# Kernel optimization log

Measured on AMD Instinct MI355X. Metric: run time of the kernel, lower is better.

Reference implementation:

```python
import jax, jax.numpy as jnp
import numpy as np

N, C, S = 2, 512, 256
SCALE = 2.0

def setup_inputs() -> dict:
    key = jax.random.key(0)
    kq, kk, kv = jax.random.split(key, 3)
    q = jax.random.normal(kq, (N, C, S), dtype=jnp.float32)
    k = jax.random.normal(kk, (N, C, S), dtype=jnp.float32)
    v = jax.random.normal(kv, (N, C, S), dtype=jnp.float32)
    return {"q": q, "k": k, "v": v}

def reference(q, k, v):
    # q: (N,C,S) -> (N,C,1,S); k: (N,C,S) -> (N,1,C,S)
    # weights[n,c,d] = -sum_s |k[n,d,s] - q[n,c,s]| / scale
    diff = jnp.abs(k[:, None, :, :] - q[:, :, None, :])  # (N,C,C,S)
    weights = -(diff / SCALE).sum(axis=-1)               # (N,C,C)
    weights = jax.nn.softmax(weights, axis=-1)
    rep = jnp.einsum('ncd,nds->ncs', weights, v)         # (N,C,S)
    return rep
```

## Files before the change

kernel.cpp:

```cpp
#include <hip/hip_runtime.h>
#include <hip/hip_bf16.h>


constexpr int N_ = 2;
constexpr int C_ = 512;
constexpr int S_ = 256;
constexpr int TC = 4;
constexpr int NW = 4;

template <int CTRL, int ROW_MASK>
__device__ __forceinline__ float dpp_add(float x) {
    int yi = __builtin_amdgcn_update_dpp(0, __float_as_int(x), CTRL, ROW_MASK, 0xf, true);
    return x + __int_as_float(yi);
}
template <int CTRL, int ROW_MASK>
__device__ __forceinline__ float dpp_max(float x) {
    int yi = __builtin_amdgcn_update_dpp(__float_as_int(x), __float_as_int(x), CTRL, ROW_MASK, 0xf, false);
    return fmaxf(x, __int_as_float(yi));
}
__device__ __forceinline__ float dpp_reduce_halves(float x) {
    x = dpp_add<0x111, 0xf>(x);
    x = dpp_add<0x112, 0xf>(x);
    x = dpp_add<0x114, 0xf>(x);
    x = dpp_add<0x118, 0xf>(x);
    x = dpp_add<0x142, 0xa>(x);
    return x;
}
__device__ __forceinline__ float wave_sum_bcast(float x) {
    x = dpp_reduce_halves(x);
    x = dpp_add<0x143, 0xc>(x);
    return __int_as_float(__builtin_amdgcn_readlane(__float_as_int(x), 63));
}
__device__ __forceinline__ float wave_max_bcast(float x) {
    x = dpp_max<0x111, 0xf>(x);
    x = dpp_max<0x112, 0xf>(x);
    x = dpp_max<0x114, 0xf>(x);
    x = dpp_max<0x118, 0xf>(x);
    x = dpp_max<0x142, 0xa>(x);
    x = dpp_max<0x143, 0xc>(x);
    return __int_as_float(__builtin_amdgcn_readlane(__float_as_int(x), 63));
}

template <int DSPLIT>
__global__ __launch_bounds__(256, 4)
void laplace_attn_main(const float* __restrict__ q,
                       const float* __restrict__ k,
                       const float* __restrict__ v,
                       float* __restrict__ ws) {
    constexpr int DH  = C_ / DSPLIT;
    constexpr int DPW = DH / NW;
    constexpr int E   = DH / 64;
    constexpr size_t PO_SZ = (size_t)N_ * C_ * DSPLIT * S_;
    constexpr size_t ST_SZ = (size_t)N_ * C_ * DSPLIT;

    const int b      = blockIdx.x;
    constexpr int per_n = (C_ / TC) * DSPLIT;
    const int n    = b / per_n;
    const int r    = b - n * per_n;
    const int half = r % DSPLIT;
    const int c0   = (r / DSPLIT) * TC;
    const int tid  = threadIdx.x;
    const int w    = tid >> 6;
    const int lane = tid & 63;

    const float* kbase = k + (size_t)n * C_ * S_;
    const float* vbase = v + (size_t)n * C_ * S_;

    float* po = ws;
    float* pm = ws + PO_SZ;
    float* pl = pm + ST_SZ;

    __shared__ float4 wt[DH];
    __shared__ float4 accs[NW][TC][64];

    const int h = lane >> 5;
    const int j = lane & 31;
    float4 qa[TC], qb[TC];
    #pragma unroll
    for (int c = 0; c < TC; ++c) {
        const float4* qr = (const float4*)(q + ((size_t)n * C_ + c0 + c) * S_);
        qa[c] = qr[2 * j];
        qb[c] = qr[2 * j + 1];
    }

    const int dw0 = half * DH + w * DPW;
    const float* kw = kbase + (size_t)dw0 * S_;

    #pragma unroll 2
    for (int g2 = 0; g2 < DPW; g2 += 2) {
        const float4* rp = (const float4*)(kw + (size_t)(g2 + h) * S_ + j * 8);
        const float4 ka = rp[0];
        const float4 kb = rp[1];
        float s0[TC], s1[TC];
        #pragma unroll
        for (int c = 0; c < TC; ++c) {
            float p = fabsf(ka.x - qa[c].x) + fabsf(ka.y - qa[c].y)
                    + fabsf(ka.z - qa[c].z) + fabsf(ka.w - qa[c].w)
                    + fabsf(kb.x - qb[c].x) + fabsf(kb.y - qb[c].y)
                    + fabsf(kb.z - qb[c].z) + fabsf(kb.w - qb[c].w);
            p = dpp_reduce_halves(p);
            s0[c] = __int_as_float(__builtin_amdgcn_readlane(__float_as_int(p), 31));
            s1[c] = __int_as_float(__builtin_amdgcn_readlane(__float_as_int(p), 63));
        }
        if (lane == 0) {
            wt[w * DPW + g2]     = make_float4(-0.5f * s0[0], -0.5f * s0[1],
                                               -0.5f * s0[2], -0.5f * s0[3]);
            wt[w * DPW + g2 + 1] = make_float4(-0.5f * s1[0], -0.5f * s1[1],
                                               -0.5f * s1[2], -0.5f * s1[3]);
        }
    }
    __syncthreads();

    {
        const float* wtf = (const float*)wt;
        float x[E];
        #pragma unroll
        for (int e = 0; e < E; ++e) x[e] = wtf[(lane + 64 * e) * 4 + w];
        float m = x[0];
        #pragma unroll
        for (int e = 1; e < E; ++e) m = fmaxf(m, x[e]);
        m = wave_max_bcast(m);
        float es[E], l = 0.f;
        #pragma unroll
        for (int e = 0; e < E; ++e) { es[e] = __expf(x[e] - m); l += es[e]; }
        l = wave_sum_bcast(l);
        float* wtm = (float*)wt;
        #pragma unroll
        for (int e = 0; e < E; ++e) wtm[(lane + 64 * e) * 4 + w] = es[e];
        if (lane == 0) {
            const size_t sidx = ((size_t)n * C_ + c0 + w) * DSPLIT + half;
            pm[sidx] = m;
            pl[sidx] = l;
        }
    }
    __syncthreads();

    float4 acc[TC];
    #pragma unroll
    for (int c = 0; c < TC; ++c) acc[c] = make_float4(0.f, 0.f, 0.f, 0.f);

    const float4* v4 = (const float4*)(vbase + (size_t)dw0 * S_);
    #pragma unroll 4
    for (int dd = 0; dd < DPW; ++dd) {
        const float4 vv = v4[dd * 64 + lane];
        const float4 ww = wt[w * DPW + dd];
        acc[0].x += ww.x * vv.x; acc[0].y += ww.x * vv.y;
        acc[0].z += ww.x * vv.z; acc[0].w += ww.x * vv.w;
        acc[1].x += ww.y * vv.x; acc[1].y += ww.y * vv.y;
        acc[1].z += ww.y * vv.z; acc[1].w += ww.y * vv.w;
        acc[2].x += ww.z * vv.x; acc[2].y += ww.z * vv.y;
        acc[2].z += ww.z * vv.z; acc[2].w += ww.z * vv.w;
        acc[3].x += ww.w * vv.x; acc[3].y += ww.w * vv.y;
        acc[3].z += ww.w * vv.z; acc[3].w += ww.w * vv.w;
    }
    #pragma unroll
    for (int c = 0; c < TC; ++c) accs[w][c][lane] = acc[c];
    __syncthreads();

    {
        const int c = w;
        float4 a  = accs[0][c][lane];
        float4 bq = accs[1][c][lane];
        float4 cc = accs[2][c][lane];
        float4 dq = accs[3][c][lane];
        float4 o;
        o.x = (a.x + bq.x) + (cc.x + dq.x);
        o.y = (a.y + bq.y) + (cc.y + dq.y);
        o.z = (a.z + bq.z) + (cc.z + dq.z);
        o.w = (a.w + bq.w) + (cc.w + dq.w);
        const size_t oidx = (((size_t)n * C_ + c0 + c) * DSPLIT + half) * S_;
        ((float4*)(po + oidx))[lane] = o;
    }
}

template <int DSPLIT>
__global__ __launch_bounds__(64)
void laplace_attn_combine(const float* __restrict__ ws,
                          float* __restrict__ out) {
    constexpr size_t PO_SZ = (size_t)N_ * C_ * DSPLIT * S_;
    constexpr size_t ST_SZ = (size_t)N_ * C_ * DSPLIT;
    const int b    = blockIdx.x;
    const int lane = threadIdx.x;

    const float* po = ws;
    const float* pm = ws + PO_SZ;
    const float* pl = pm + ST_SZ;

    float m[DSPLIT], l[DSPLIT];
    #pragma unroll
    for (int hh = 0; hh < DSPLIT; ++hh) {
        m[hh] = pm[(size_t)b * DSPLIT + hh];
        l[hh] = pl[(size_t)b * DSPLIT + hh];
    }
    float M = m[0];
    #pragma unroll
    for (int hh = 1; hh < DSPLIT; ++hh) M = fmaxf(M, m[hh]);
    float den = 0.f, a[DSPLIT];
    #pragma unroll
    for (int hh = 0; hh < DSPLIT; ++hh) { a[hh] = __expf(m[hh] - M); den += a[hh] * l[hh]; }
    const float inv = 1.f / den;

    float4 rsum = make_float4(0.f, 0.f, 0.f, 0.f);
    #pragma unroll
    for (int hh = 0; hh < DSPLIT; ++hh) {
        const float4 o = ((const float4*)(po + ((size_t)b * DSPLIT + hh) * S_))[lane];
        rsum.x += a[hh] * o.x;
        rsum.y += a[hh] * o.y;
        rsum.z += a[hh] * o.z;
        rsum.w += a[hh] * o.w;
    }
    float4 rr;
    rr.x = rsum.x * inv; rr.y = rsum.y * inv;
    rr.z = rsum.z * inv; rr.w = rsum.w * inv;
    ((float4*)(out + (size_t)b * S_))[lane] = rr;
}

extern "C" void kernel_launch(void* const* d_in, const int* in_sizes, int n_in,
                              void* d_out, int out_size, void* d_ws, size_t ws_size,
                              hipStream_t stream) {
    const float* q = (const float*)d_in[0];
    const float* k = (const float*)d_in[1];
    const float* v = (const float*)d_in[2];
    float* out = (float*)d_out;
    float* ws  = (float*)d_ws;

    constexpr size_t NEED4 =
        ((size_t)N_ * C_ * 4 * S_ + 2 * (size_t)N_ * C_ * 4) * sizeof(float);

    if (ws_size >= NEED4) {
        laplace_attn_main<4><<<dim3(N_ * (C_ / TC) * 4), dim3(256), 0, stream>>>(q, k, v, ws);
        laplace_attn_combine<4><<<dim3(N_ * C_), dim3(64), 0, stream>>>(ws, out);
    } else {
        laplace_attn_main<2><<<dim3(N_ * (C_ / TC) * 2), dim3(256), 0, stream>>>(q, k, v, ws);
        laplace_attn_combine<2><<<dim3(N_ * C_), dim3(64), 0, stream>>>(ws, out);
    }
}
```

Measured before the change: 77.29 us.

## Double query tile to 8 rows and split keys eight ways

Each block now handles 8 query rows instead of 4, so each loaded K and V row is reused across twice as many outputs. The key dimension is split into 8 chunks of 64 instead of 4, which keeps the grid at 1024 blocks and gives one softmax element per lane. The template and workspace-size fallback are removed, so the kernel always assumes a workspace large enough for 8 partial outputs. The trade-off is more accumulator registers (32 floats), more cross-lane reductions per K row, and a heavier combine step that reads 8 partials per output row.

```diff
diff --git a/kernel.cpp b/kernel.cpp
--- a/kernel.cpp
+++ b/kernel.cpp
@@ -5,8 +5,14 @@
 constexpr int N_ = 2;
 constexpr int C_ = 512;
 constexpr int S_ = 256;
-constexpr int TC = 4;
+constexpr int TC = 8;
 constexpr int NW = 4;
+constexpr int DSPLIT = 8;
+constexpr int DH  = C_ / DSPLIT;
+constexpr int DPW = DH / NW;
+
+constexpr size_t PO_SZ = (size_t)N_ * C_ * DSPLIT * S_;
+constexpr size_t ST_SZ = (size_t)N_ * C_ * DSPLIT;
 
 template <int CTRL, int ROW_MASK>
 __device__ __forceinline__ float dpp_add(float x) {
@@ -41,20 +47,13 @@
     return __int_as_float(__builtin_amdgcn_readlane(__float_as_int(x), 63));
 }
 
-template <int DSPLIT>
 __global__ __launch_bounds__(256, 4)
 void laplace_attn_main(const float* __restrict__ q,
                        const float* __restrict__ k,
                        const float* __restrict__ v,
                        float* __restrict__ ws) {
-    constexpr int DH  = C_ / DSPLIT;
-    constexpr int DPW = DH / NW;
-    constexpr int E   = DH / 64;
-    constexpr size_t PO_SZ = (size_t)N_ * C_ * DSPLIT * S_;
-    constexpr size_t ST_SZ = (size_t)N_ * C_ * DSPLIT;
-
-    const int b      = blockIdx.x;
     constexpr int per_n = (C_ / TC) * DSPLIT;
+    const int b    = blockIdx.x;
     const int n    = b / per_n;
     const int r    = b - n * per_n;
     const int half = r % DSPLIT;
@@ -70,7 +69,7 @@
     float* pm = ws + PO_SZ;
     float* pl = pm + ST_SZ;
 
-    __shared__ float4 wt[DH];
+    __shared__ float4 wt[DH][2];
     __shared__ float4 accs[NW][TC][64];
 
     const int h = lane >> 5;
@@ -91,46 +90,40 @@
         const float4* rp = (const float4*)(kw + (size_t)(g2 + h) * S_ + j * 8);
         const float4 ka = rp[0];
         const float4 kb = rp[1];
-        float s0[TC], s1[TC];
+        float vals[TC];
         #pragma unroll
         for (int c = 0; c < TC; ++c) {
             float p = fabsf(ka.x - qa[c].x) + fabsf(ka.y - qa[c].y)
                     + fabsf(ka.z - qa[c].z) + fabsf(ka.w - qa[c].w)
                     + fabsf(kb.x - qb[c].x) + fabsf(kb.y - qb[c].y)
                     + fabsf(kb.z - qb[c].z) + fabsf(kb.w - qb[c].w);
-            p = dpp_reduce_halves(p);
-            s0[c] = __int_as_float(__builtin_amdgcn_readlane(__float_as_int(p), 31));
-            s1[c] = __int_as_float(__builtin_amdgcn_readlane(__float_as_int(p), 63));
+            vals[c] = dpp_reduce_halves(p);
         }
-        if (lane == 0) {
-            wt[w * DPW + g2]     = make_float4(-0.5f * s0[0], -0.5f * s0[1],
-                                               -0.5f * s0[2], -0.5f * s0[3]);
-            wt[w * DPW + g2 + 1] = make_float4(-0.5f * s1[0], -0.5f * s1[1],
-                                               -0.5f * s1[2], -0.5f * s1[3]);
+        if ((lane & 31) == 31) {
+            const int row = w * DPW + g2 + h;
+            wt[row][0] = make_float4(-0.5f * vals[0], -0.5f * vals[1],
+                                     -0.5f * vals[2], -0.5f * vals[3]);
+            wt[row][1] = make_float4(-0.5f * vals[4], -0.5f * vals[5],
+                                     -0.5f * vals[6], -0.5f * vals[7]);
         }
     }
     __syncthreads();
 
     {
-        const float* wtf = (const float*)wt;
-        float x[E];
+        float* wtf = (float*)wt;
         #pragma unroll
-        for (int e = 0; e < E; ++e) x[e] = wtf[(lane + 64 * e) * 4 + w];
-        float m = x[0];
-        #pragma unroll
-        for (int e = 1; e < E; ++e) m = fmaxf(m, x[e]);
-        m = wave_max_bcast(m);
-        float es[E], l = 0.f;
-        #pragma unroll
-        for (int e = 0; e < E; ++e) { es[e] = __expf(x[e] - m); l += es[e]; }
-        l = wave_sum_bcast(l);
-        float* wtm = (float*)wt;
-        #pragma unroll
-        for (int e = 0; e < E; ++e) wtm[(lane + 64 * e) * 4 + w] = es[e];
-        if (lane == 0) {
-            const size_t sidx = ((size_t)n * C_ + c0 + w) * DSPLIT + half;
-            pm[sidx] = m;
-            pl[sidx] = l;
+        for (int cc = 0; cc < 2; ++cc) {
+            const int c = 2 * w + cc;
+            const float x = wtf[lane * 8 + c];
+            const float m = wave_max_bcast(x);
+            const float e = __expf(x - m);
+            const float l = wave_sum_bcast(e);
+            wtf[lane * 8 + c] = e;
+            if (lane == 0) {
+                const size_t sidx = ((size_t)n * C_ + c0 + c) * DSPLIT + half;
+                pm[sidx] = m;
+                pl[sidx] = l;
+            }
         }
     }
     __syncthreads();
@@ -143,42 +136,49 @@
     #pragma unroll 4
     for (int dd = 0; dd < DPW; ++dd) {
         const float4 vv = v4[dd * 64 + lane];
-        const float4 ww = wt[w * DPW + dd];
-        acc[0].x += ww.x * vv.x; acc[0].y += ww.x * vv.y;
-        acc[0].z += ww.x * vv.z; acc[0].w += ww.x * vv.w;
-        acc[1].x += ww.y * vv.x; acc[1].y += ww.y * vv.y;
-        acc[1].z += ww.y * vv.z; acc[1].w += ww.y * vv.w;
-        acc[2].x += ww.z * vv.x; acc[2].y += ww.z * vv.y;
-        acc[2].z += ww.z * vv.z; acc[2].w += ww.z * vv.w;
-        acc[3].x += ww.w * vv.x; acc[3].y += ww.w * vv.y;
-        acc[3].z += ww.w * vv.z; acc[3].w += ww.w * vv.w;
+        const float4 w0 = wt[w * DPW + dd][0];
+        const float4 w1 = wt[w * DPW + dd][1];
+        acc[0].x += w0.x * vv.x; acc[0].y += w0.x * vv.y;
+        acc[0].z += w0.x * vv.z; acc[0].w += w0.x * vv.w;
+        acc[1].x += w0.y * vv.x; acc[1].y += w0.y * vv.y;
+        acc[1].z += w0.y * vv.z; acc[1].w += w0.y * vv.w;
+        acc[2].x += w0.z * vv.x; acc[2].y += w0.z * vv.y;
+        acc[2].z += w0.z * vv.z; acc[2].w += w0.z * vv.w;
+        acc[3].x += w0.w * vv.x; acc[3].y += w0.w * vv.y;
+        acc[3].z += w0.w * vv.z; acc[3].w += w0.w * vv.w;
+        acc[4].x += w1.x * vv.x; acc[4].y += w1.x * vv.y;
+        acc[4].z += w1.x * vv.z; acc[4].w += w1.x * vv.w;
+        acc[5].x += w1.y * vv.x; acc[5].y += w1.y * vv.y;
+        acc[5].z += w1.y * vv.z; acc[5].w += w1.y * vv.w;
+        acc[6].x += w1.z * vv.x; acc[6].y += w1.z * vv.y;
+        acc[6].z += w1.z * vv.z; acc[6].w += w1.z * vv.w;
+        acc[7].x += w1.w * vv.x; acc[7].y += w1.w * vv.y;
+        acc[7].z += w1.w * vv.z; acc[7].w += w1.w * vv.w;
     }
     #pragma unroll
     for (int c = 0; c < TC; ++c) accs[w][c][lane] = acc[c];
     __syncthreads();
 
-    {
-        const int c = w;
-        float4 a  = accs[0][c][lane];
-        float4 bq = accs[1][c][lane];
-        float4 cc = accs[2][c][lane];
-        float4 dq = accs[3][c][lane];
+    #pragma unroll
+    for (int cc = 0; cc < 2; ++cc) {
+        const int c = w + NW * cc;
+        const float4 a0 = accs[0][c][lane];
+        const float4 a1 = accs[1][c][lane];
+        const float4 a2 = accs[2][c][lane];
+        const float4 a3 = accs[3][c][lane];
         float4 o;
-        o.x = (a.x + bq.x) + (cc.x + dq.x);
-        o.y = (a.y + bq.y) + (cc.y + dq.y);
-        o.z = (a.z + bq.z) + (cc.z + dq.z);
-        o.w = (a.w + bq.w) + (cc.w + dq.w);
+        o.x = (a0.x + a1.x) + (a2.x + a3.x);
+        o.y = (a0.y + a1.y) + (a2.y + a3.y);
+        o.z = (a0.z + a1.z) + (a2.z + a3.z);
+        o.w = (a0.w + a1.w) + (a2.w + a3.w);
         const size_t oidx = (((size_t)n * C_ + c0 + c) * DSPLIT + half) * S_;
         ((float4*)(po + oidx))[lane] = o;
     }
 }
 
-template <int DSPLIT>
 __global__ __launch_bounds__(64)
 void laplace_attn_combine(const float* __restrict__ ws,
                           float* __restrict__ out) {
-    constexpr size_t PO_SZ = (size_t)N_ * C_ * DSPLIT * S_;
-    constexpr size_t ST_SZ = (size_t)N_ * C_ * DSPLIT;
     const int b    = blockIdx.x;
     const int lane = threadIdx.x;
 
@@ -224,14 +224,6 @@
     float* out = (float*)d_out;
     float* ws  = (float*)d_ws;
 
-    constexpr size_t NEED4 =
-        ((size_t)N_ * C_ * 4 * S_ + 2 * (size_t)N_ * C_ * 4) * sizeof(float);
-
-    if (ws_size >= NEED4) {
-        laplace_attn_main<4><<<dim3(N_ * (C_ / TC) * 4), dim3(256), 0, stream>>>(q, k, v, ws);
-        laplace_attn_combine<4><<<dim3(N_ * C_), dim3(64), 0, stream>>>(ws, out);
-    } else {
-        laplace_attn_main<2><<<dim3(N_ * (C_ / TC) * 2), dim3(256), 0, stream>>>(q, k, v, ws);
-        laplace_attn_combine<2><<<dim3(N_ * C_), dim3(64), 0, stream>>>(ws, out);
-    }
-}
+    laplace_attn_main<<<dim3(N_ * (C_ / TC) * DSPLIT), dim3(256), 0, stream>>>(q, k, v, ws);
+    laplace_attn_combine<<<dim3(N_ * C_), dim3(64), 0, stream>>>(ws, out);
+}
```

Measured after the change: 81.13 us. 1.05x slower.
